# Optimization experiments

Hardware: AMD Instinct MI355X
Metric: run time of the kernel (lower is better)

The kernel has to match this reference:

```python
import jax, jax.numpy as jnp
import numpy as np

N, D = 8192, 128
TEMPERATURE = 0.5


def _l2_normalize(x, eps):
    # matches F.normalize / utils.sim_matrix norm clamping
    n = jnp.linalg.norm(x, axis=1, keepdims=True)
    return x / jnp.maximum(n, eps)


def setup_inputs() -> dict:
    key = jax.random.key(0)
    k1, k2, k3 = jax.random.split(key, 3)
    nodes = jax.random.normal(k1, (N, D), dtype=jnp.float32)
    pair_nodes = jax.random.normal(k2, (N, D), dtype=jnp.float32)
    nodes_labels = jax.random.randint(k3, (N,), 0, 20).astype(jnp.int64)
    # standard NT-Xent self-mask: exclude diagonal from the denominator
    mask = jnp.eye(N, dtype=bool)
    return {"nodes": nodes, "pair_nodes": pair_nodes,
            "nodes_labels": nodes_labels, "mask": mask}


def reference(nodes, pair_nodes, nodes_labels, mask):
    # z, z_p: F.normalize(..., dim=1), eps=1e-12
    z = _l2_normalize(nodes, 1e-12)
    z_p = _l2_normalize(pair_nodes, 1e-12)
    # pairwise cosine similarity [N, N] == z @ z_p.T since rows are unit-norm
    positive_similarity = jnp.einsum('id,jd->ij', z, z_p)
    nominator = jnp.exp(positive_similarity / TEMPERATURE)  # [N, N]
    # utils.sim_matrix(nodes, nodes): cosine sim matrix with eps=1e-8 clamp
    zn = _l2_normalize(nodes, 1e-8)
    similarity_matrix = jnp.einsum('id,jd->ij', zn, zn)  # [N, N]
    denominator = (~mask).astype(jnp.float32) * jnp.exp(similarity_matrix / TEMPERATURE)
    den_sum = jnp.sum(denominator, axis=1)  # [N]
    # torch broadcasting: [N,N] / [N] divides along the LAST axis (columns)
    loss_partial = -jnp.log(nominator / den_sum[None, :])
    loss = jnp.sum(loss_partial) / nodes.shape[0]
    return loss
```

## Files before the change

### kernel.cpp

```cpp
#include <hip/hip_runtime.h>

#define N 8192
#define D 128
#define NT 64
#define PRESCALE 1.6986435984699773f

typedef __bf16 bf16;
typedef __bf16 bf16x8 __attribute__((ext_vector_type(8)));
typedef float f32x4 __attribute__((ext_vector_type(4)));

#define ZBF_OFF 0
#define DEN_OFF (N * D * 2)
#define S_OFF   (DEN_OFF + N * 4)
#define SP_OFF  (S_OFF + 512)

__global__ __launch_bounds__(256) void norm_kernel(
    const float* __restrict__ nodes, const float* __restrict__ pair,
    bf16* __restrict__ zbf, float* __restrict__ svec, float* __restrict__ spvec)
{
    __shared__ float red[4][128];
    const int tid = threadIdx.x;
    const int lane = tid & 63, wave = tid >> 6;
    const int g = lane & 15, q = lane >> 4;
    const bool isPair = blockIdx.x >= 512;
    const float* src = isPair ? pair : nodes;
    const int row = (blockIdx.x & 511) * 16 + wave * 4 + q;

    const float4 x0 = *(const float4*)(src + row * D + g * 8);
    const float4 x1 = *(const float4*)(src + row * D + g * 8 + 4);
    float ss = x0.x * x0.x + x0.y * x0.y + x0.z * x0.z + x0.w * x0.w
             + x1.x * x1.x + x1.y * x1.y + x1.z * x1.z + x1.w * x1.w;
    #pragma unroll
    for (int m = 1; m <= 8; m <<= 1) ss += __shfl_xor(ss, m, 64);
    const float nrm = sqrtf(ss);
    const float inv12 = 1.f / fmaxf(nrm, 1e-12f);

    float a[8] = { x0.x * inv12, x0.y * inv12, x0.z * inv12, x0.w * inv12,
                   x1.x * inv12, x1.y * inv12, x1.z * inv12, x1.w * inv12 };

    if (!isPair) {
        const float sc = PRESCALE / fmaxf(nrm, 1e-8f);
        bf16x8 pk;
        pk[0] = (bf16)(x0.x * sc); pk[1] = (bf16)(x0.y * sc);
        pk[2] = (bf16)(x0.z * sc); pk[3] = (bf16)(x0.w * sc);
        pk[4] = (bf16)(x1.x * sc); pk[5] = (bf16)(x1.y * sc);
        pk[6] = (bf16)(x1.z * sc); pk[7] = (bf16)(x1.w * sc);
        *(bf16x8*)(zbf + row * D + g * 8) = pk;
    }

    #pragma unroll
    for (int k = 0; k < 8; ++k) {
        a[k] += __shfl_xor(a[k], 16, 64);
        a[k] += __shfl_xor(a[k], 32, 64);
    }
    if (q == 0) {
        #pragma unroll
        for (int k = 0; k < 8; ++k) red[wave][g * 8 + k] = a[k];
    }
    __syncthreads();
    if (tid < 128) {
        float* dst = isPair ? spvec : svec;
        atomicAdd(&dst[tid], red[0][tid] + red[1][tid] + red[2][tid] + red[3][tid]);
    }
}

#define LDP 80

__global__ __launch_bounds__(256) void gemm_kernel(
    const bf16* __restrict__ zbf, float* __restrict__ den)
{
    __shared__ bf16 As[128 * LDP];
    __shared__ bf16 Bs[128 * LDP];
    __shared__ float rowacc[128];
    __shared__ float colacc[128];

    int b = blockIdx.x;
    int ti = (int)((2.0 * NT + 1.0 - sqrt((2.0 * NT + 1.0) * (2.0 * NT + 1.0) - 8.0 * (double)b)) * 0.5);
    while (ti > 0 && ti * (2 * NT + 1 - ti) / 2 > b) --ti;
    while ((ti + 1) * (2 * NT - ti) / 2 <= b) ++ti;
    const int tj = ti + (b - ti * (2 * NT + 1 - ti) / 2);
    const bool diag = (ti == tj);

    const int tid  = threadIdx.x;
    const int lane = tid & 63, wave = tid >> 6;
    const int wm = wave >> 1, wn = wave & 1;
    const int quad = lane >> 4, c = lane & 15;
    const int ibase = ti * 128;
    const int jbase = tj * 128;

    if (tid < 128) { rowacc[tid] = 0.f; colacc[tid] = 0.f; }

    f32x4 acc[4][4];
    #pragma unroll
    for (int i = 0; i < 4; ++i)
        #pragma unroll
        for (int j = 0; j < 4; ++j) acc[i][j] = (f32x4){0.f, 0.f, 0.f, 0.f};

    uint4 va[4], vb[4];
    #pragma unroll
    for (int i = 0; i < 4; ++i) {
        const int chunk = tid + 256 * i;
        const int row = chunk >> 3, c8 = (chunk & 7) * 8;
        va[i] = *(const uint4*)(zbf + (ibase + row) * D + c8);
        vb[i] = *(const uint4*)(zbf + (jbase + row) * D + c8);
    }
    #pragma unroll
    for (int i = 0; i < 4; ++i) {
        const int chunk = tid + 256 * i;
        const int row = chunk >> 3, c8 = (chunk & 7) * 8;
        *(uint4*)(&As[row * LDP + c8]) = va[i];
        *(uint4*)(&Bs[row * LDP + c8]) = vb[i];
    }
    #pragma unroll
    for (int i = 0; i < 4; ++i) {
        const int chunk = tid + 256 * i;
        const int row = chunk >> 3, c8 = (chunk & 7) * 8;
        va[i] = *(const uint4*)(zbf + (ibase + row) * D + 64 + c8);
        vb[i] = *(const uint4*)(zbf + (jbase + row) * D + 64 + c8);
    }
    __syncthreads();

    #pragma unroll
    for (int kh = 0; kh < 2; ++kh) {
        #pragma unroll
        for (int ks = 0; ks < 2; ++ks) {
            const int kk = ks * 32;
            bf16x8 af[4], bfr[4];
            #pragma unroll
            for (int mi = 0; mi < 4; ++mi)
                af[mi] = *(const bf16x8*)(&As[(wm * 64 + mi * 16 + c) * LDP + kk + quad * 8]);
            #pragma unroll
            for (int ni = 0; ni < 4; ++ni)
                bfr[ni] = *(const bf16x8*)(&Bs[(wn * 64 + ni * 16 + c) * LDP + kk + quad * 8]);
            #pragma unroll
            for (int mi = 0; mi < 4; ++mi)
                #pragma unroll
                for (int ni = 0; ni < 4; ++ni)
                    acc[mi][ni] = __builtin_amdgcn_mfma_f32_16x16x32_bf16(
                        af[mi], bfr[ni], acc[mi][ni], 0, 0, 0);
        }
        if (kh == 0) {
            __syncthreads();
            #pragma unroll
            for (int i = 0; i < 4; ++i) {
                const int chunk = tid + 256 * i;
                const int row = chunk >> 3, c8 = (chunk & 7) * 8;
                *(uint4*)(&As[row * LDP + c8]) = va[i];
                *(uint4*)(&Bs[row * LDP + c8]) = vb[i];
            }
            __syncthreads();
        }
    }

    float rowp[4][4];
    float colp[4];
    #pragma unroll
    for (int mi = 0; mi < 4; ++mi)
        #pragma unroll
        for (int r = 0; r < 4; ++r) rowp[mi][r] = 0.f;
    #pragma unroll
    for (int ni = 0; ni < 4; ++ni) colp[ni] = 0.f;

    #pragma unroll
    for (int mi = 0; mi < 4; ++mi) {
        const int lrow0 = wm * 64 + mi * 16 + quad * 4;
        #pragma unroll
        for (int ni = 0; ni < 4; ++ni) {
            const int lcol = wn * 64 + ni * 16 + c;
            const f32x4 cv = acc[mi][ni];
            #pragma unroll
            for (int r = 0; r < 4; ++r) {
                float e = __builtin_amdgcn_exp2f(cv[r]);
                if (diag && (lrow0 + r == lcol)) e = 0.f;
                rowp[mi][r] += e;
                colp[ni]    += e;
            }
        }
    }

    #pragma unroll
    for (int mi = 0; mi < 4; ++mi)
        #pragma unroll
        for (int r = 0; r < 4; ++r) {
            #pragma unroll
            for (int m = 1; m <= 8; m <<= 1)
                rowp[mi][r] += __shfl_xor(rowp[mi][r], m, 64);
        }
    if (c == 0) {
        #pragma unroll
        for (int mi = 0; mi < 4; ++mi)
            #pragma unroll
            for (int r = 0; r < 4; ++r)
                atomicAdd(&rowacc[wm * 64 + mi * 16 + quad * 4 + r], rowp[mi][r]);
    }

    if (!diag) {
        #pragma unroll
        for (int ni = 0; ni < 4; ++ni) {
            colp[ni] += __shfl_xor(colp[ni], 16, 64);
            colp[ni] += __shfl_xor(colp[ni], 32, 64);
        }
        if (quad == 0) {
            #pragma unroll
            for (int ni = 0; ni < 4; ++ni)
                atomicAdd(&colacc[wn * 64 + ni * 16 + c], colp[ni]);
        }
    }

    __syncthreads();
    if (tid < 128) {
        atomicAdd(&den[ibase + tid], rowacc[tid]);
        if (!diag) atomicAdd(&den[jbase + tid], colacc[tid]);
    }
}

__global__ __launch_bounds__(256) void final_kernel(
    const float* __restrict__ den, const float* __restrict__ s,
    const float* __restrict__ sp, float* __restrict__ out)
{
    __shared__ float red[4];
    const int tid = threadIdx.x;
    float v = 0.f;
    for (int j = tid; j < N; j += 256) v += logf(den[j]);
    if (tid < 128) v -= s[tid] * sp[tid] * (1.f / 4096.f);
    #pragma unroll
    for (int m = 32; m >= 1; m >>= 1) v += __shfl_xor(v, m, 64);
    if ((tid & 63) == 0) red[tid >> 6] = v;
    __syncthreads();
    if (tid == 0) out[0] = red[0] + red[1] + red[2] + red[3];
}

extern "C" void kernel_launch(void* const* d_in, const int* in_sizes, int n_in,
                              void* d_out, int out_size, void* d_ws, size_t ws_size,
                              hipStream_t stream)
{
    const float* nodes = (const float*)d_in[0];
    const float* pair  = (const float*)d_in[1];

    char*  ws  = (char*)d_ws;
    bf16*  zbf = (bf16*)(ws + ZBF_OFF);
    float* den = (float*)(ws + DEN_OFF);
    float* s   = (float*)(ws + S_OFF);
    float* sp  = (float*)(ws + SP_OFF);

    hipMemsetAsync(ws + DEN_OFF, 0, N * 4 + 1024, stream);

    hipLaunchKernelGGL(norm_kernel, dim3(1024), dim3(256), 0, stream,
                       nodes, pair, zbf, s, sp);
    hipLaunchKernelGGL(gemm_kernel, dim3(NT * (NT + 1) / 2), dim3(256), 0, stream,
                       zbf, den);
    hipLaunchKernelGGL(final_kernel, dim3(1), dim3(256), 0, stream,
                       den, s, sp, (float*)d_out);
}
```

Measured before the change: 361.7 us.

## Load GEMM tiles directly into swizzled LDS and parallelize final reduction

```diff
diff --git a/kernel.cpp b/kernel.cpp
--- a/kernel.cpp
+++ b/kernel.cpp
@@ -13,6 +13,12 @@
 #define DEN_OFF (N * D * 2)
 #define S_OFF   (DEN_OFF + N * 4)
 #define SP_OFF  (S_OFF + 512)
+
+__device__ __forceinline__ void load_lds16(const bf16* g, bf16* l) {
+    __builtin_amdgcn_global_load_lds(
+        (const __attribute__((address_space(1))) unsigned int*)g,
+        (__attribute__((address_space(3))) unsigned int*)l, 16, 0, 0);
+}
 
 __global__ __launch_bounds__(256) void norm_kernel(
     const float* __restrict__ nodes, const float* __restrict__ pair,
@@ -64,15 +70,13 @@
     }
 }
 
-#define LDP 80
-
 __global__ __launch_bounds__(256) void gemm_kernel(
     const bf16* __restrict__ zbf, float* __restrict__ den)
 {
-    __shared__ bf16 As[128 * LDP];
-    __shared__ bf16 Bs[128 * LDP];
-    __shared__ float rowacc[128];
-    __shared__ float colacc[128];
+    __shared__ bf16 As[128 * 128];
+    __shared__ bf16 Bs[128 * 128];
+    __shared__ float rowacc[2][128];
+    __shared__ float colacc[2][128];
 
     int b = blockIdx.x;
     int ti = (int)((2.0 * NT + 1.0 - sqrt((2.0 * NT + 1.0) * (2.0 * NT + 1.0) - 8.0 * (double)b)) * 0.5);
@@ -88,7 +92,29 @@
     const int ibase = ti * 128;
     const int jbase = tj * 128;
 
-    if (tid < 128) { rowacc[tid] = 0.f; colacc[tid] = 0.f; }
+    {
+        const int rsub = lane >> 4;
+        const int slot = lane & 15;
+        #pragma unroll
+        for (int i = 0; i < 8; ++i) {
+            const int blk4 = wave * 8 + i;
+            const int row  = blk4 * 4 + rsub;
+            const int cc   = slot ^ (row & 15);
+            load_lds16(zbf + (ibase + row) * D + cc * 8, As + blk4 * 512 + lane * 8);
+        }
+        if (!diag) {
+            #pragma unroll
+            for (int i = 0; i < 8; ++i) {
+                const int blk4 = wave * 8 + i;
+                const int row  = blk4 * 4 + rsub;
+                const int cc   = slot ^ (row & 15);
+                load_lds16(zbf + (jbase + row) * D + cc * 8, Bs + blk4 * 512 + lane * 8);
+            }
+        }
+    }
+    __syncthreads();
+
+    const bf16* Bp = diag ? As : Bs;
 
     f32x4 acc[4][4];
     #pragma unroll
@@ -96,60 +122,26 @@
         #pragma unroll
         for (int j = 0; j < 4; ++j) acc[i][j] = (f32x4){0.f, 0.f, 0.f, 0.f};
 
-    uint4 va[4], vb[4];
-    #pragma unroll
-    for (int i = 0; i < 4; ++i) {
-        const int chunk = tid + 256 * i;
-        const int row = chunk >> 3, c8 = (chunk & 7) * 8;
-        va[i] = *(const uint4*)(zbf + (ibase + row) * D + c8);
-        vb[i] = *(const uint4*)(zbf + (jbase + row) * D + c8);
-    }
-    #pragma unroll
-    for (int i = 0; i < 4; ++i) {
-        const int chunk = tid + 256 * i;
-        const int row = chunk >> 3, c8 = (chunk & 7) * 8;
-        *(uint4*)(&As[row * LDP + c8]) = va[i];
-        *(uint4*)(&Bs[row * LDP + c8]) = vb[i];
-    }
-    #pragma unroll
-    for (int i = 0; i < 4; ++i) {
-        const int chunk = tid + 256 * i;
-        const int row = chunk >> 3, c8 = (chunk & 7) * 8;
-        va[i] = *(const uint4*)(zbf + (ibase + row) * D + 64 + c8);
-        vb[i] = *(const uint4*)(zbf + (jbase + row) * D + 64 + c8);
-    }
-    __syncthreads();
-
-    #pragma unroll
-    for (int kh = 0; kh < 2; ++kh) {
-        #pragma unroll
-        for (int ks = 0; ks < 2; ++ks) {
-            const int kk = ks * 32;
-            bf16x8 af[4], bfr[4];
-            #pragma unroll
-            for (int mi = 0; mi < 4; ++mi)
-                af[mi] = *(const bf16x8*)(&As[(wm * 64 + mi * 16 + c) * LDP + kk + quad * 8]);
+    #pragma unroll
+    for (int ks = 0; ks < 4; ++ks) {
+        const int s = ks * 4 + quad;
+        bf16x8 af[4], bfr[4];
+        #pragma unroll
+        for (int mi = 0; mi < 4; ++mi) {
+            const int r = wm * 64 + mi * 16 + c;
+            af[mi] = *(const bf16x8*)(As + r * 128 + ((s ^ c) * 8));
+        }
+        #pragma unroll
+        for (int ni = 0; ni < 4; ++ni) {
+            const int r = wn * 64 + ni * 16 + c;
+            bfr[ni] = *(const bf16x8*)(Bp + r * 128 + ((s ^ c) * 8));
+        }
+        #pragma unroll
+        for (int mi = 0; mi < 4; ++mi)
             #pragma unroll
             for (int ni = 0; ni < 4; ++ni)
-                bfr[ni] = *(const bf16x8*)(&Bs[(wn * 64 + ni * 16 + c) * LDP + kk + quad * 8]);
-            #pragma unroll
-            for (int mi = 0; mi < 4; ++mi)
-                #pragma unroll
-                for (int ni = 0; ni < 4; ++ni)
-                    acc[mi][ni] = __builtin_amdgcn_mfma_f32_16x16x32_bf16(
-                        af[mi], bfr[ni], acc[mi][ni], 0, 0, 0);
-        }
-        if (kh == 0) {
-            __syncthreads();
-            #pragma unroll
-            for (int i = 0; i < 4; ++i) {
-                const int chunk = tid + 256 * i;
-                const int row = chunk >> 3, c8 = (chunk & 7) * 8;
-                *(uint4*)(&As[row * LDP + c8]) = va[i];
-                *(uint4*)(&Bs[row * LDP + c8]) = vb[i];
-            }
-            __syncthreads();
-        }
+                acc[mi][ni] = __builtin_amdgcn_mfma_f32_16x16x32_bf16(
+                    af[mi], bfr[ni], acc[mi][ni], 0, 0, 0);
     }
 
     float rowp[4][4];
@@ -191,7 +183,7 @@
         for (int mi = 0; mi < 4; ++mi)
             #pragma unroll
             for (int r = 0; r < 4; ++r)
-                atomicAdd(&rowacc[wm * 64 + mi * 16 + quad * 4 + r], rowp[mi][r]);
+                rowacc[wn][wm * 64 + mi * 16 + quad * 4 + r] = rowp[mi][r];
     }
 
     if (!diag) {
@@ -203,14 +195,14 @@
         if (quad == 0) {
             #pragma unroll
             for (int ni = 0; ni < 4; ++ni)
-                atomicAdd(&colacc[wn * 64 + ni * 16 + c], colp[ni]);
+                colacc[wm][wn * 64 + ni * 16 + c] = colp[ni];
         }
     }
 
     __syncthreads();
     if (tid < 128) {
-        atomicAdd(&den[ibase + tid], rowacc[tid]);
-        if (!diag) atomicAdd(&den[jbase + tid], colacc[tid]);
+        atomicAdd(&den[ibase + tid], rowacc[0][tid] + rowacc[1][tid]);
+        if (!diag) atomicAdd(&den[jbase + tid], colacc[0][tid] + colacc[1][tid]);
     }
 }
 
@@ -219,15 +211,16 @@
     const float* __restrict__ sp, float* __restrict__ out)
 {
     __shared__ float red[4];
-    const int tid = threadIdx.x;
-    float v = 0.f;
-    for (int j = tid; j < N; j += 256) v += logf(den[j]);
-    if (tid < 128) v -= s[tid] * sp[tid] * (1.f / 4096.f);
+    const int tid = threadIdx.x, lane = tid & 63, wave = tid >> 6;
+    const float2 d2 = *(const float2*)(den + blockIdx.x * 512 + tid * 2);
+    float v = logf(d2.x) + logf(d2.y);
+    if (blockIdx.x == 0 && tid < 128)
+        v -= s[tid] * sp[tid] * (1.f / 4096.f);
     #pragma unroll
     for (int m = 32; m >= 1; m >>= 1) v += __shfl_xor(v, m, 64);
-    if ((tid & 63) == 0) red[tid >> 6] = v;
-    __syncthreads();
-    if (tid == 0) out[0] = red[0] + red[1] + red[2] + red[3];
+    if (lane == 0) red[wave] = v;
+    __syncthreads();
+    if (tid == 0) atomicAdd(out, red[0] + red[1] + red[2] + red[3]);
 }
 
 extern "C" void kernel_launch(void* const* d_in, const int* in_sizes, int n_in,
@@ -244,11 +237,12 @@
     float* sp  = (float*)(ws + SP_OFF);
 
     hipMemsetAsync(ws + DEN_OFF, 0, N * 4 + 1024, stream);
+    hipMemsetAsync(d_out, 0, 4, stream);
 
     hipLaunchKernelGGL(norm_kernel, dim3(1024), dim3(256), 0, stream,
                        nodes, pair, zbf, s, sp);
     hipLaunchKernelGGL(gemm_kernel, dim3(NT * (NT + 1) / 2), dim3(256), 0, stream,
                        zbf, den);
-    hipLaunchKernelGGL(final_kernel, dim3(1), dim3(256), 0, stream,
+    hipLaunchKernelGGL(final_kernel, dim3(16), dim3(256), 0, stream,
                        den, s, sp, (float*)d_out);
 }
```

After: 339.9 us. 1.06x faster.
